# Optimization experiments

Measured on AMD Instinct MI355X. Metric: run time of the kernel, lower is better.

## Reference

```python
import jax, jax.numpy as jnp
import numpy as np

B, S, D, H = 2, 2048, 1024, 16
DH = D // H


def setup_inputs() -> dict:
    key = jax.random.key(0)
    ks = jax.random.split(key, 7)
    scale = 1.0 / np.sqrt(D)
    queries = jax.random.normal(ks[0], (B, S, D), dtype=jnp.float32)
    keys_ = jax.random.normal(ks[1], (B, S, D), dtype=jnp.float32)
    values = jax.random.normal(ks[2], (B, S, D), dtype=jnp.float32)
    mask = jnp.tril(jnp.ones((S, S), dtype=jnp.int32))[None, None]  # causal [1,1,S,S]
    Wq = jax.random.normal(ks[3], (D, D), dtype=jnp.float32) * scale
    Wk = jax.random.normal(ks[4], (D, D), dtype=jnp.float32) * scale
    Wv = jax.random.normal(ks[5], (D, D), dtype=jnp.float32) * scale
    Wo = jax.random.normal(ks[6], (D, D), dtype=jnp.float32) * scale
    return {"queries": queries, "keys": keys_, "values": values, "mask": mask,
            "Wq": Wq, "Wk": Wk, "Wv": Wv, "Wo": Wo}


def reference(queries, keys, values, mask, Wq, Wk, Wv, Wo):
    # linear projections (nn.Linear, no bias): x @ W.T
    def split_heads(x, W):
        return (x @ W.T).reshape(B, -1, H, DH).transpose(0, 2, 1, 3)  # [B,H,S,DH]

    q = split_heads(queries, Wq)
    k = split_heads(keys, Wk)
    v = split_heads(values, Wv)

    scores = jnp.einsum('bhqd,bhkd->bhqk', q, k) / jnp.sqrt(jnp.float32(DH))
    scores = jnp.where(mask == 0, jnp.float32(-jnp.inf), scores)
    weights = jax.nn.softmax(scores, axis=-1)  # dropout p=0.0 -> identity
    out = jnp.einsum('bhqk,bhkd->bhqd', weights, v)
    out = out.transpose(0, 2, 1, 3).reshape(B, -1, D)
    return out @ Wo.T
```

## Files before the change

### kernel.cpp

```cpp
#include <hip/hip_runtime.h>
#include <hip/hip_bf16.h>


typedef unsigned short u16;
typedef __attribute__((ext_vector_type(8))) short bf16x8;
typedef __attribute__((ext_vector_type(4))) float f32x4;
typedef __attribute__((ext_vector_type(4))) short s16x4;

#define DEVI static __device__ __forceinline__
#define SCL 0.18033688011112042f
#define LDSW 40
#define GLDS(g, l) __builtin_amdgcn_global_load_lds( \
    (const __attribute__((address_space(1))) unsigned*)(g), \
    (__attribute__((address_space(3))) unsigned*)(l), 16, 0, 0)

DEVI u16 f2bf(float f) {
  __hip_bfloat16 h = __float2bfloat16(f);
  union { __hip_bfloat16 h; u16 u; } c; c.h = h;
  return c.u;
}

DEVI bf16x8 cvt8(f32x4 a, f32x4 b) {
  bf16x8 r;
  r[0] = (short)f2bf(a[0]); r[1] = (short)f2bf(a[1]);
  r[2] = (short)f2bf(a[2]); r[3] = (short)f2bf(a[3]);
  r[4] = (short)f2bf(b[0]); r[5] = (short)f2bf(b[1]);
  r[6] = (short)f2bf(b[2]); r[7] = (short)f2bf(b[3]);
  return r;
}

template <int F32>
DEVI void load_pair(f32x4* lo, f32x4* hi, bf16x8* bb, const void* P,
                    size_t o0, size_t o1) {
  if constexpr (F32) {
    const float* p0 = (const float*)P + o0;
    const float* p1 = (const float*)P + o1;
    lo[0] = *(const f32x4*)p0; hi[0] = *(const f32x4*)(p0 + 4);
    lo[1] = *(const f32x4*)p1; hi[1] = *(const f32x4*)(p1 + 4);
  } else {
    bb[0] = *(const bf16x8*)((const u16*)P + o0);
    bb[1] = *(const bf16x8*)((const u16*)P + o1);
  }
}

template <int F32>
DEVI void finish_pair(f32x4* lo, f32x4* hi, bf16x8* bb, u16* dst, int le0, int le1) {
  if constexpr (F32) { bb[0] = cvt8(lo[0], hi[0]); bb[1] = cvt8(lo[1], hi[1]); }
  *(bf16x8*)(dst + le0) = bb[0];
  *(bf16x8*)(dst + le1) = bb[1];
}

template <int MODE, int O32>
DEVI void epilogue(f32x4 (&acc)[4][4], void* C, int tileM, int tileN,
                   int wr, int wc, int lr, int lg, float oscale) {
  constexpr int N = 1024;
  if constexpr (MODE == 0) {
#pragma unroll
    for (int m = 0; m < 4; ++m) {
      const int row0 = tileM + wr + m * 16 + lg * 4;
#pragma unroll
      for (int n = 0; n < 4; ++n) {
        const int col = tileN + wc + n * 16 + lr;
#pragma unroll
        for (int j = 0; j < 4; ++j) {
          if constexpr (O32)
            ((float*)C)[(size_t)(row0 + j) * N + col] = acc[m][n][j] * oscale;
          else
            ((u16*)C)[(size_t)(row0 + j) * N + col] = f2bf(acc[m][n][j] * oscale);
        }
      }
    }
  } else if constexpr (MODE == 1) {
    u16* Cv = (u16*)C;
#pragma unroll
    for (int m = 0; m < 4; ++m) {
      const int row0 = tileM + wr + m * 16 + lg * 4;
      const int bb = row0 >> 11, s0 = row0 & 2047;
#pragma unroll
      for (int n = 0; n < 4; ++n) {
        const int col = tileN + wc + n * 16 + lr;
        s16x4 pk;
#pragma unroll
        for (int j = 0; j < 4; ++j) pk[j] = (short)f2bf(acc[m][n][j]);
        *(s16x4*)(Cv + ((size_t)(col + (bb << 10)) << 11) + s0) = pk;
      }
    }
  } else {
    u16* Cv = (u16*)C;
#pragma unroll
    for (int m = 0; m < 4; ++m) {
      const int row0 = tileM + wr + m * 16 + lg * 4;
      const int bb = row0 >> 11, s0 = row0 & 2047;
#pragma unroll
      for (int n = 0; n < 4; ++n) {
        const int col = tileN + wc + n * 16 + lr;
        const size_t base = ((size_t)((bb << 4) + (col >> 6)) * 2048 + s0) * 64 + (col & 63);
#pragma unroll
        for (int j = 0; j < 4; ++j)
          Cv[base + (size_t)j * 64] = f2bf(acc[m][n][j]);
      }
    }
  }
}

template <int A32, int W32, int MODE, int O32>
DEVI void gemm_core(u16* sA0, u16* sA1, u16* sB0, u16* sB1,
                    const void* A, const void* W, void* C,
                    int tileM, int tileN, float oscale) {
  constexpr int K = 1024;
  const int tid = threadIdx.x;
  const int lane = tid & 63;
  const int wave = tid >> 6;
  const int wr = (wave >> 1) * 64;
  const int wc = (wave & 1) * 64;
  const int lr = lane & 15, lg = lane >> 4;

  f32x4 acc[4][4] = {};

  const int e0 = tid * 8;
  const int e1 = 2048 + tid * 8;
  const int r0 = e0 >> 5, c0 = e0 & 31;
  const int r1 = e1 >> 5, c1 = e1 & 31;
  const int le0 = r0 * LDSW + c0;
  const int le1 = r1 * LDSW + c1;
  const size_t oA0 = (size_t)(tileM + r0) * K + c0;
  const size_t oA1 = (size_t)(tileM + r1) * K + c1;
  const size_t oB0 = (size_t)(tileN + r0) * K + c0;
  const size_t oB1 = (size_t)(tileN + r1) * K + c1;

  f32x4 aeLo[2], aeHi[2], aoLo[2], aoHi[2], wLo[2], wHi[2];
  bf16x8 aeB[2], aoB[2], wB[2];

  load_pair<A32>(aeLo, aeHi, aeB, A, oA0, oA1);
  load_pair<W32>(wLo, wHi, wB, W, oB0, oB1);
  finish_pair<A32>(aeLo, aeHi, aeB, sA0, le0, le1);
  finish_pair<W32>(wLo, wHi, wB, sB0, le0, le1);
  load_pair<A32>(aoLo, aoHi, aoB, A, oA0 + 32, oA1 + 32);
  __syncthreads();

#pragma unroll 1
  for (int it = 0; it < 16; ++it) {
    const int kE = it * 64;
    {
      bf16x8 af[4], bfr[4];
#pragma unroll
      for (int m = 0; m < 4; ++m)
        af[m] = *(const bf16x8*)(sA0 + (wr + m * 16 + lr) * LDSW + lg * 8);
#pragma unroll
      for (int n = 0; n < 4; ++n)
        bfr[n] = *(const bf16x8*)(sB0 + (wc + n * 16 + lr) * LDSW + lg * 8);
      if (it < 15) load_pair<A32>(aeLo, aeHi, aeB, A, oA0 + kE + 64, oA1 + kE + 64);
      load_pair<W32>(wLo, wHi, wB, W, oB0 + kE + 32, oB1 + kE + 32);
#pragma unroll
      for (int m = 0; m < 4; ++m)
#pragma unroll
        for (int n = 0; n < 4; ++n)
          acc[m][n] = __builtin_amdgcn_mfma_f32_16x16x32_bf16(af[m], bfr[n], acc[m][n], 0, 0, 0);
      finish_pair<A32>(aoLo, aoHi, aoB, sA1, le0, le1);
      finish_pair<W32>(wLo, wHi, wB, sB1, le0, le1);
      __syncthreads();
    }
    {
      bf16x8 af[4], bfr[4];
#pragma unroll
      for (int m = 0; m < 4; ++m)
        af[m] = *(const bf16x8*)(sA1 + (wr + m * 16 + lr) * LDSW + lg * 8);
#pragma unroll
      for (int n = 0; n < 4; ++n)
        bfr[n] = *(const bf16x8*)(sB1 + (wc + n * 16 + lr) * LDSW + lg * 8);
      if (it < 15) {
        load_pair<A32>(aoLo, aoHi, aoB, A, oA0 + kE + 96, oA1 + kE + 96);
        load_pair<W32>(wLo, wHi, wB, W, oB0 + kE + 64, oB1 + kE + 64);
      }
#pragma unroll
      for (int m = 0; m < 4; ++m)
#pragma unroll
        for (int n = 0; n < 4; ++n)
          acc[m][n] = __builtin_amdgcn_mfma_f32_16x16x32_bf16(af[m], bfr[n], acc[m][n], 0, 0, 0);
      if (it < 15) {
        finish_pair<A32>(aeLo, aeHi, aeB, sA0, le0, le1);
        finish_pair<W32>(wLo, wHi, wB, sB0, le0, le1);
      }
      __syncthreads();
    }
  }
  epilogue<MODE, O32>(acc, C, tileM, tileN, wr, wc, lr, lg, oscale);
}

DEVI void tile_remap(int& tileM, int& tileN) {
  const int i = blockIdx.x + 8 * blockIdx.y;
  const int c = i & 7, s = i >> 3;
  tileM = (c * 4 + (s & 3)) * 128;
  tileN = (s >> 2) * 128;
}

template <int IN32>
__global__ void __launch_bounds__(256, 3)
gemm_qkv(const void* __restrict__ q, const void* __restrict__ wq, u16* __restrict__ Qp,
         const void* __restrict__ k, const void* __restrict__ wk, u16* __restrict__ Kh,
         const void* __restrict__ v, const void* __restrict__ wv, u16* __restrict__ Vt) {
  __shared__ __align__(16) u16 sA[2][128 * LDSW];
  __shared__ __align__(16) u16 sB[2][128 * LDSW];
  int tileM, tileN;
  tile_remap(tileM, tileN);
  if (blockIdx.z == 0)
    gemm_core<IN32, IN32, 0, 0>(sA[0], sA[1], sB[0], sB[1], q, wq, Qp, tileM, tileN, SCL);
  else if (blockIdx.z == 1)
    gemm_core<IN32, IN32, 2, 0>(sA[0], sA[1], sB[0], sB[1], k, wk, Kh, tileM, tileN, 1.f);
  else
    gemm_core<IN32, IN32, 1, 0>(sA[0], sA[1], sB[0], sB[1], v, wv, Vt, tileM, tileN, 1.f);
}

template <int W32, int O32>
__global__ void __launch_bounds__(256, 3)
gemm_out(const u16* __restrict__ A, const void* __restrict__ W, void* __restrict__ C) {
  __shared__ __align__(16) u16 sA[2][128 * LDSW];
  __shared__ __align__(16) u16 sB[2][128 * LDSW];
  int tileM, tileN;
  tile_remap(tileM, tileN);
  gemm_core<0, W32, 0, O32>(sA[0], sA[1], sB[0], sB[1], A, W, C, tileM, tileN, 1.f);
}


DEVI void stage_klds(const u16* __restrict__ Kb, const u16* __restrict__ Vb,
                     u16* sKb, u16* sVb, int kt, int w, int lane) {
  const int kr = lane >> 3;
  const int kg = (lane & 7) ^ kr;
  const u16* gk = Kb + (size_t)(kt + w * 16 + kr) * 64 + kg * 8;
  const int vr = lane >> 2;
  const int vg = (lane & 3) ^ ((lane >> 3) & 3);
  const u16* gv = Vb + (size_t)(w * 32 + vr) * 2048 + kt + vg * 8;
  u16* dk = sKb + w * 1024;
  u16* dv = sVb + w * 1024;
  GLDS(gk, dk);
  GLDS(gk + 8 * 64, dk + 512);
  GLDS(gv, dv);
  GLDS(gv + (size_t)16 * 2048, dv + 512);
}

__global__ void __launch_bounds__(128, 3)
attn_kernel(const u16* Qp, const u16* __restrict__ Kh,
            const u16* __restrict__ Vt, u16* AO) {
  __shared__ __align__(16) u16 sK[3][2048];
  __shared__ __align__(16) u16 sV[3][2048];
  const int tid = threadIdx.x;
  const int lane = tid & 63;
  const int w = tid >> 6;
  const int lr = lane & 15;
  const int lg = lane >> 4;

  const int id = blockIdx.x;
  const int xcd = id & 7;
  const int slot = id >> 3;
  const int bh = xcd * 4 + (slot & 3);
  const int band = 63 - (slot >> 2);
  const int b = bh >> 4;
  const int h = bh & 15;
  const int r0 = band * 32;

  const u16* Kb = Kh + (size_t)bh * 2048 * 64;
  const u16* Vb = Vt + (size_t)bh * 64 * 2048;

  const int qrow = r0 + w * 16 + lr;
  const u16* Qw = Qp + ((size_t)(b * 2048 + qrow) << 10) + h * 64;
  const bf16x8 qf0 = *(const bf16x8*)(Qw + lg * 8);
  const bf16x8 qf1 = *(const bf16x8*)(Qw + 32 + lg * 8);

  f32x4 o[4] = {};
  float mr = -INFINITY, ls = 0.f;
  const int nt = band + 1;

  stage_klds(Kb, Vb, sK[0], sV[0], 0, w, lane);

#pragma unroll 1
  for (int t = 0; t < nt; ++t) {
    if (t + 1 < nt) {
      const int bi = (t + 1) % 3;
      stage_klds(Kb, Vb, sK[bi], sV[bi], (t + 1) * 32, w, lane);
      asm volatile("s_waitcnt vmcnt(4)" ::: "memory");
    } else {
      asm volatile("s_waitcnt vmcnt(0)" ::: "memory");
    }
    asm volatile("s_barrier" ::: "memory");
    __builtin_amdgcn_s_setprio(1);

    {
      const int bi = t % 3;
      const u16* sKb = sK[bi];
      const u16* sVb = sV[bi];
      const int sw = lr & 7;
      const bf16x8 kf0 = *(const bf16x8*)(sKb + lr * 64 + ((lg ^ sw) * 8));
      const bf16x8 kf1 = *(const bf16x8*)(sKb + lr * 64 + (((4 + lg) ^ sw) * 8));
      const bf16x8 kf2 = *(const bf16x8*)(sKb + (16 + lr) * 64 + ((lg ^ sw) * 8));
      const bf16x8 kf3 = *(const bf16x8*)(sKb + (16 + lr) * 64 + (((4 + lg) ^ sw) * 8));

      const f32x4 z = {};
      f32x4 s0 = __builtin_amdgcn_mfma_f32_16x16x32_bf16(kf0, qf0, z, 0, 0, 0);
      s0 = __builtin_amdgcn_mfma_f32_16x16x32_bf16(kf1, qf1, s0, 0, 0, 0);
      f32x4 s1 = __builtin_amdgcn_mfma_f32_16x16x32_bf16(kf2, qf0, z, 0, 0, 0);
      s1 = __builtin_amdgcn_mfma_f32_16x16x32_bf16(kf3, qf1, s1, 0, 0, 0);

      float p[8];
#pragma unroll
      for (int j = 0; j < 4; ++j) { p[j] = s0[j]; p[4 + j] = s1[j]; }
      if (t == nt - 1) {
        const int kt0 = t * 32;
#pragma unroll
        for (int j = 0; j < 4; ++j) {
          if (kt0 + lg * 4 + j > qrow)      p[j] = -INFINITY;
          if (kt0 + 16 + lg * 4 + j > qrow) p[4 + j] = -INFINITY;
        }
      }

      const float tm = fmaxf(fmaxf(fmaxf(p[0], p[1]), fmaxf(p[2], p[3])),
                             fmaxf(fmaxf(p[4], p[5]), fmaxf(p[6], p[7])));
      if (!__all(tm <= mr + 11.5f)) {
        float tr_ = fmaxf(tm, __shfl_xor(tm, 16));
        tr_ = fmaxf(tr_, __shfl_xor(tr_, 32));
        const float mn = fmaxf(mr, tr_);
        const float fac = exp2f(mr - mn);
        mr = mn;
        ls *= fac;
#pragma unroll
        for (int j = 0; j < 4; ++j) {
          const float fj = __shfl(fac, lg * 4 + j);
#pragma unroll
          for (int d = 0; d < 4; ++d) o[d][j] *= fj;
        }
      }

#pragma unroll
      for (int i = 0; i < 8; ++i) p[i] = exp2f(p[i] - mr);
      ls += ((p[0] + p[1]) + (p[2] + p[3])) + ((p[4] + p[5]) + (p[6] + p[7]));

      bf16x8 pa;
#pragma unroll
      for (int i = 0; i < 8; ++i) pa[i] = (short)f2bf(p[i]);

      const int s2 = (lr >> 1) & 3;
#pragma unroll
      for (int d = 0; d < 4; ++d) {
        const u16* vrow = sVb + (16 * d + lr) * 32;
        const s16x4 v0 = *(const s16x4*)(vrow + (((lg >> 1) ^ s2) * 8) + (lg & 1) * 4);
        const s16x4 v1 = *(const s16x4*)(vrow + ((((lg >> 1) + 2) ^ s2) * 8) + (lg & 1) * 4);
        bf16x8 vf;
        vf[0] = v0[0]; vf[1] = v0[1]; vf[2] = v0[2]; vf[3] = v0[3];
        vf[4] = v1[0]; vf[5] = v1[1]; vf[6] = v1[2]; vf[7] = v1[3];
        o[d] = __builtin_amdgcn_mfma_f32_16x16x32_bf16(pa, vf, o[d], 0, 0, 0);
      }
    }
    __builtin_amdgcn_s_setprio(0);
  }

  float lt = ls + __shfl_xor(ls, 16);
  lt += __shfl_xor(lt, 32);
  const size_t orow = (size_t)(b * 2048 + r0 + w * 16 + lg * 4);
#pragma unroll
  for (int j = 0; j < 4; ++j) {
    const float inv = 1.0f / __shfl(lt, lg * 4 + j);
#pragma unroll
    for (int d = 0; d < 4; ++d)
      AO[(orow + j) * 1024 + h * 64 + 16 * d + lr] = f2bf(o[d][j] * inv);
  }
}

static int bytes_per_elem(void* p, long long n, void* pnext) {
  if (pnext) {
    ptrdiff_t d = (char*)pnext - (char*)p;
    if (d == n * 2) return 2;
    if (d == n * 4) return 4;
  }
  size_t sz = 0;
  if (hipMemPtrGetInfo(p, &sz) == hipSuccess && sz >= (size_t)(n * 2)) {
    if (sz < (size_t)(n * 4)) return 2;
    if (sz <= (size_t)(n * 8)) return 4;
  }
  return 4;
}

extern "C" void kernel_launch(void* const* d_in, const int* in_sizes, int n_in,
                              void* d_out, int out_size, void* d_ws, size_t ws_size,
                              hipStream_t stream) {
  void* q  = d_in[0];
  void* k  = d_in[1];
  void* v  = d_in[2];
  void* wq = d_in[4];
  void* wk = d_in[5];
  void* wv = d_in[6];
  void* wo = d_in[7];

  const int in32 = bytes_per_elem(q, in_sizes[0], k) == 4;
  const int w32  = bytes_per_elem(wq, in_sizes[4], wk) == 4;
  const int o32  = bytes_per_elem(d_out, out_size, nullptr) == 4;

  const size_t SZ = (size_t)4096 * 1024;
  u16* Qp = (u16*)d_ws;
  u16* Kh = Qp + SZ;
  u16* Vt = (u16*)d_out;
  u16* AO = Qp;

  if (in32)
    gemm_qkv<1><<<dim3(8, 32, 3), 256, 0, stream>>>(q, wq, Qp, k, wk, Kh, v, wv, Vt);
  else
    gemm_qkv<0><<<dim3(8, 32, 3), 256, 0, stream>>>(q, wq, Qp, k, wk, Kh, v, wv, Vt);

  attn_kernel<<<dim3(2048), 128, 0, stream>>>(Qp, Kh, Vt, AO);

  if (w32) {
    if (o32) gemm_out<1, 1><<<dim3(8, 32), 256, 0, stream>>>(AO, wo, d_out);
    else     gemm_out<1, 0><<<dim3(8, 32), 256, 0, stream>>>(AO, wo, d_out);
  } else {
    if (o32) gemm_out<0, 1><<<dim3(8, 32), 256, 0, stream>>>(AO, wo, d_out);
    else     gemm_out<0, 0><<<dim3(8, 32), 256, 0, stream>>>(AO, wo, d_out);
  }
}
```

Baseline: 130.9 us.

## Pre-convert weights to swizzled bf16 tiles and stage them via global_load_lds

Adds a conversion kernel that turns Wq/Wk/Wv/Wo into bf16 laid out in per-tile, XOR-swizzled 128x32 blocks. The GEMM cores then load weight tiles straight into LDS with async global_load_lds and explicit vmcnt waits, instead of loading fp32 through registers and converting every time. This is meant to cut register pressure, conversion ALU work and global traffic in the GEMM inner loop. The cost is two extra kernel launches per call, extra workspace traffic, and reuse of the output and Kh buffers as scratch, which depends on buffer lifetimes being correct.

New measurement: 125.0 us. -4.6%, faster.

```diff
diff --git a/kernel.cpp b/kernel.cpp
--- a/kernel.cpp
+++ b/kernel.cpp
@@ -27,6 +27,16 @@
   r[4] = (short)f2bf(b[0]); r[5] = (short)f2bf(b[1]);
   r[6] = (short)f2bf(b[2]); r[7] = (short)f2bf(b[3]);
   return r;
+}
+
+template <int F32>
+DEVI bf16x8 lda8(const void* base, size_t off) {
+  if constexpr (!F32) {
+    return *(const bf16x8*)((const u16*)base + off);
+  } else {
+    const float* p = (const float*)base + off;
+    return cvt8(*(const f32x4*)p, *(const f32x4*)(p + 4));
+  }
 }
 
 template <int F32>
@@ -50,6 +60,10 @@
   *(bf16x8*)(dst + le1) = bb[1];
 }
 
+DEVI void vwait4() { asm volatile("s_waitcnt vmcnt(4)" ::: "memory"); }
+DEVI void vwait2() { asm volatile("s_waitcnt vmcnt(2)" ::: "memory"); }
+DEVI void vwait0() { asm volatile("s_waitcnt vmcnt(0)" ::: "memory"); }
+
 template <int MODE, int O32>
 DEVI void epilogue(f32x4 (&acc)[4][4], void* C, int tileM, int tileN,
                    int wr, int wc, int lr, int lg, float oscale) {
@@ -103,9 +117,23 @@
   }
 }
 
-template <int A32, int W32, int MODE, int O32>
-DEVI void gemm_core(u16* sA0, u16* sA1, u16* sB0, u16* sB1,
-                    const void* A, const void* W, void* C,
+template <int F32>
+__global__ void __launch_bounds__(256)
+cvt_w3(const void* w0, const void* w1, const void* w2,
+       u16* o0, u16* o1, u16* o2) {
+  const int y = blockIdx.y;
+  const void* w = (y == 0) ? w0 : ((y == 1) ? w1 : w2);
+  u16* o = (y == 0) ? o0 : ((y == 1) ? o1 : o2);
+  const int r = blockIdx.x * 256 + threadIdx.x;
+  const int p = r >> 14, t = (r >> 9) & 31, row = (r >> 2) & 127, g = r & 3;
+  const int col = t * 32 + ((g ^ ((row >> 1) & 3)) << 3);
+  const size_t src = ((size_t)(p * 128 + row) << 10) + col;
+  *(bf16x8*)(o + (size_t)r * 8) = lda8<F32>(w, src);
+}
+
+template <int A32, int MODE, int O32>
+DEVI void gemm_core(u16* sA0, u16* sA1, u16* sW0, u16* sW1,
+                    const void* A, const u16* Wb, void* C,
                     int tileM, int tileN, float oscale) {
   constexpr int K = 1024;
   const int tid = threadIdx.x;
@@ -125,65 +153,76 @@
   const int le1 = r1 * LDSW + c1;
   const size_t oA0 = (size_t)(tileM + r0) * K + c0;
   const size_t oA1 = (size_t)(tileM + r1) * K + c1;
-  const size_t oB0 = (size_t)(tileN + r0) * K + c0;
-  const size_t oB1 = (size_t)(tileN + r1) * K + c1;
-
-  f32x4 aeLo[2], aeHi[2], aoLo[2], aoHi[2], wLo[2], wHi[2];
-  bf16x8 aeB[2], aoB[2], wB[2];
-
-  load_pair<A32>(aeLo, aeHi, aeB, A, oA0, oA1);
-  load_pair<W32>(wLo, wHi, wB, W, oB0, oB1);
-  finish_pair<A32>(aeLo, aeHi, aeB, sA0, le0, le1);
-  finish_pair<W32>(wLo, wHi, wB, sB0, le0, le1);
-  load_pair<A32>(aoLo, aoHi, aoB, A, oA0 + 32, oA1 + 32);
+
+  const u16* WB = Wb + ((size_t)(tileN >> 7) * 32) * 4096 + tid * 8;
+  u16* dW0 = sW0 + (tid & ~63) * 8 / 64 * 512 / 8;
+  dW0 = sW0 + wave * 512;
+  u16* dW1 = sW1 + wave * 512;
+#define STAGE_W(tt, dst) { GLDS(WB + (size_t)(tt) * 4096, dst); \
+                           GLDS(WB + (size_t)(tt) * 4096 + 2048, (dst) + 2048); }
+
+  f32x4 eLo[2], eHi[2], oLo[2], oHi[2];
+  bf16x8 eB[2], oB[2];
+
+  load_pair<A32>(eLo, eHi, eB, A, oA0, oA1);
+  STAGE_W(0, dW0);
+  finish_pair<A32>(eLo, eHi, eB, sA0, le0, le1);
+  load_pair<A32>(oLo, oHi, oB, A, oA0 + 32, oA1 + 32);
+  if constexpr (A32) vwait4(); else vwait2();
   __syncthreads();
 
 #pragma unroll 1
   for (int it = 0; it < 16; ++it) {
-    const int kE = it * 64;
     {
+      const int tE = it * 2;
+      STAGE_W(tE + 1, dW1);
       bf16x8 af[4], bfr[4];
 #pragma unroll
       for (int m = 0; m < 4; ++m)
         af[m] = *(const bf16x8*)(sA0 + (wr + m * 16 + lr) * LDSW + lg * 8);
 #pragma unroll
-      for (int n = 0; n < 4; ++n)
-        bfr[n] = *(const bf16x8*)(sB0 + (wc + n * 16 + lr) * LDSW + lg * 8);
-      if (it < 15) load_pair<A32>(aeLo, aeHi, aeB, A, oA0 + kE + 64, oA1 + kE + 64);
-      load_pair<W32>(wLo, wHi, wB, W, oB0 + kE + 32, oB1 + kE + 32);
+      for (int n = 0; n < 4; ++n) {
+        const int row = wc + n * 16 + lr;
+        bfr[n] = *(const bf16x8*)(sW0 + row * 32 + ((lg ^ ((row >> 1) & 3)) << 3));
+      }
+      if (it < 15) load_pair<A32>(eLo, eHi, eB, A, oA0 + (tE + 2) * 32, oA1 + (tE + 2) * 32);
 #pragma unroll
       for (int m = 0; m < 4; ++m)
 #pragma unroll
         for (int n = 0; n < 4; ++n)
           acc[m][n] = __builtin_amdgcn_mfma_f32_16x16x32_bf16(af[m], bfr[n], acc[m][n], 0, 0, 0);
-      finish_pair<A32>(aoLo, aoHi, aoB, sA1, le0, le1);
-      finish_pair<W32>(wLo, wHi, wB, sB1, le0, le1);
+      finish_pair<A32>(oLo, oHi, oB, sA1, le0, le1);
+      if (it < 15) { if constexpr (A32) vwait4(); else vwait2(); } else vwait0();
       __syncthreads();
     }
     {
+      const int tO = it * 2 + 1;
+      if (it < 15) STAGE_W(tO + 1, dW0);
       bf16x8 af[4], bfr[4];
 #pragma unroll
       for (int m = 0; m < 4; ++m)
         af[m] = *(const bf16x8*)(sA1 + (wr + m * 16 + lr) * LDSW + lg * 8);
 #pragma unroll
-      for (int n = 0; n < 4; ++n)
-        bfr[n] = *(const bf16x8*)(sB1 + (wc + n * 16 + lr) * LDSW + lg * 8);
-      if (it < 15) {
-        load_pair<A32>(aoLo, aoHi, aoB, A, oA0 + kE + 96, oA1 + kE + 96);
-        load_pair<W32>(wLo, wHi, wB, W, oB0 + kE + 64, oB1 + kE + 64);
-      }
+      for (int n = 0; n < 4; ++n) {
+        const int row = wc + n * 16 + lr;
+        bfr[n] = *(const bf16x8*)(sW1 + row * 32 + ((lg ^ ((row >> 1) & 3)) << 3));
+      }
+      if (it < 15) load_pair<A32>(oLo, oHi, oB, A, oA0 + (tO + 2) * 32, oA1 + (tO + 2) * 32);
 #pragma unroll
       for (int m = 0; m < 4; ++m)
 #pragma unroll
         for (int n = 0; n < 4; ++n)
           acc[m][n] = __builtin_amdgcn_mfma_f32_16x16x32_bf16(af[m], bfr[n], acc[m][n], 0, 0, 0);
       if (it < 15) {
-        finish_pair<A32>(aeLo, aeHi, aeB, sA0, le0, le1);
-        finish_pair<W32>(wLo, wHi, wB, sB0, le0, le1);
+        finish_pair<A32>(eLo, eHi, eB, sA0, le0, le1);
+        if constexpr (A32) vwait4(); else vwait2();
+      } else {
+        vwait0();
       }
       __syncthreads();
     }
   }
+#undef STAGE_W
   epilogue<MODE, O32>(acc, C, tileM, tileN, wr, wc, lr, lg, oscale);
 }
 
@@ -196,31 +235,30 @@
 
 template <int IN32>
 __global__ void __launch_bounds__(256, 3)
-gemm_qkv(const void* __restrict__ q, const void* __restrict__ wq, u16* __restrict__ Qp,
-         const void* __restrict__ k, const void* __restrict__ wk, u16* __restrict__ Kh,
-         const void* __restrict__ v, const void* __restrict__ wv, u16* __restrict__ Vt) {
+gemm_qkv(const void* __restrict__ q, const u16* __restrict__ WqB, u16* __restrict__ Qp,
+         const void* __restrict__ k, const u16* __restrict__ WkB, u16* __restrict__ Kh,
+         const void* __restrict__ v, const u16* __restrict__ WvB, u16* __restrict__ Vt) {
   __shared__ __align__(16) u16 sA[2][128 * LDSW];
-  __shared__ __align__(16) u16 sB[2][128 * LDSW];
+  __shared__ __align__(16) u16 sW[2][128 * 32];
   int tileM, tileN;
   tile_remap(tileM, tileN);
   if (blockIdx.z == 0)
-    gemm_core<IN32, IN32, 0, 0>(sA[0], sA[1], sB[0], sB[1], q, wq, Qp, tileM, tileN, SCL);
+    gemm_core<IN32, 0, 0>(sA[0], sA[1], sW[0], sW[1], q, WqB, Qp, tileM, tileN, SCL);
   else if (blockIdx.z == 1)
-    gemm_core<IN32, IN32, 2, 0>(sA[0], sA[1], sB[0], sB[1], k, wk, Kh, tileM, tileN, 1.f);
+    gemm_core<IN32, 2, 0>(sA[0], sA[1], sW[0], sW[1], k, WkB, Kh, tileM, tileN, 1.f);
   else
-    gemm_core<IN32, IN32, 1, 0>(sA[0], sA[1], sB[0], sB[1], v, wv, Vt, tileM, tileN, 1.f);
-}
-
-template <int W32, int O32>
+    gemm_core<IN32, 1, 0>(sA[0], sA[1], sW[0], sW[1], v, WvB, Vt, tileM, tileN, 1.f);
+}
+
+template <int O32>
 __global__ void __launch_bounds__(256, 3)
-gemm_out(const u16* __restrict__ A, const void* __restrict__ W, void* __restrict__ C) {
+gemm_out(const u16* __restrict__ A, const u16* __restrict__ WoB, void* __restrict__ C) {
   __shared__ __align__(16) u16 sA[2][128 * LDSW];
-  __shared__ __align__(16) u16 sB[2][128 * LDSW];
+  __shared__ __align__(16) u16 sW[2][128 * 32];
   int tileM, tileN;
   tile_remap(tileM, tileN);
-  gemm_core<0, W32, 0, O32>(sA[0], sA[1], sB[0], sB[1], A, W, C, tileM, tileN, 1.f);
-}
-
+  gemm_core<0, 0, O32>(sA[0], sA[1], sW[0], sW[1], A, WoB, C, tileM, tileN, 1.f);
+}
 
 DEVI void stage_klds(const u16* __restrict__ Kb, const u16* __restrict__ Vb,
                      u16* sKb, u16* sVb, int kt, int w, int lane) {
@@ -394,23 +432,29 @@
   const int o32  = bytes_per_elem(d_out, out_size, nullptr) == 4;
 
   const size_t SZ = (size_t)4096 * 1024;
+  const size_t WZ = (size_t)1024 * 1024;
   u16* Qp = (u16*)d_ws;
   u16* Kh = Qp + SZ;
   u16* Vt = (u16*)d_out;
   u16* AO = Qp;
+  u16* WqB = Vt + SZ;
+  u16* WkB = WqB + WZ;
+  u16* WvB = WkB + WZ;
+  u16* WoB = Kh;
+
+  if (w32) cvt_w3<1><<<dim3(512, 3), 256, 0, stream>>>(wq, wk, wv, WqB, WkB, WvB);
+  else     cvt_w3<0><<<dim3(512, 3), 256, 0, stream>>>(wq, wk, wv, WqB, WkB, WvB);
 
   if (in32)
-    gemm_qkv<1><<<dim3(8, 32, 3), 256, 0, stream>>>(q, wq, Qp, k, wk, Kh, v, wv, Vt);
+    gemm_qkv<1><<<dim3(8, 32, 3), 256, 0, stream>>>(q, WqB, Qp, k, WkB, Kh, v, WvB, Vt);
   else
-    gemm_qkv<0><<<dim3(8, 32, 3), 256, 0, stream>>>(q, wq, Qp, k, wk, Kh, v, wv, Vt);
+    gemm_qkv<0><<<dim3(8, 32, 3), 256, 0, stream>>>(q, WqB, Qp, k, WkB, Kh, v, WvB, Vt);
 
   attn_kernel<<<dim3(2048), 128, 0, stream>>>(Qp, Kh, Vt, AO);
 
-  if (w32) {
-    if (o32) gemm_out<1, 1><<<dim3(8, 32), 256, 0, stream>>>(AO, wo, d_out);
-    else     gemm_out<1, 0><<<dim3(8, 32), 256, 0, stream>>>(AO, wo, d_out);
-  } else {
-    if (o32) gemm_out<0, 1><<<dim3(8, 32), 256, 0, stream>>>(AO, wo, d_out);
-    else     gemm_out<0, 0><<<dim3(8, 32), 256, 0, stream>>>(AO, wo, d_out);
-  }
-}
+  if (w32) cvt_w3<1><<<dim3(512, 1), 256, 0, stream>>>(wo, wo, wo, WoB, WoB, WoB);
+  else     cvt_w3<0><<<dim3(512, 1), 256, 0, stream>>>(wo, wo, wo, WoB, WoB, WoB);
+
+  if (o32) gemm_out<1><<<dim3(8, 32), 256, 0, stream>>>(AO, WoB, d_out);
+  else     gemm_out<0><<<dim3(8, 32), 256, 0, stream>>>(AO, WoB, d_out);
+}
```
